# Kernel optimization log

Hardware: AMD Instinct MI355X
Metric: run time of the kernel (lower is better)

The kernel has to match this reference:

```python
import jax, jax.numpy as jnp
import numpy as np

D = 768
B = 32
N = 768


def setup_inputs() -> dict:
    key = jax.random.key(0)
    k1, k2, k3, k4 = jax.random.split(key, 4)
    stdv = 1.0 / np.sqrt(D)
    X = jax.random.normal(k1, (B, N, D), dtype=jnp.float32)
    adj = jax.random.uniform(k2, (B, N, N), dtype=jnp.float32)
    W_l = jax.random.uniform(k3, (D, D), dtype=jnp.float32, minval=-stdv, maxval=stdv)
    W_l1 = jax.random.uniform(k4, (D, D), dtype=jnp.float32, minval=-stdv, maxval=stdv)
    return {"X": X, "adj": adj, "W_l": W_l, "W_l1": W_l1}


def _row_normalize(adj):
    # rowsum^-1 with inf -> 0 (rows summing to zero stay zero)
    rowsum = adj.sum(axis=-1, keepdims=True)  # [B, N, 1]
    r_inv = jnp.where(rowsum == 0, 0.0, 1.0 / rowsum)
    return adj * r_inv


def reference(X, adj, W_l, W_l1):
    # X: [B, N, D], adj: [B, N, N]
    adj_n = _row_normalize(adj)
    e1 = jnp.einsum('bnd,de->bne', X, W_l1)        # message transform
    e11 = jnp.einsum('bnm,bmd->bnd', adj_n, e1)    # aggregate
    X1 = jnp.einsum('bnd,de->bne', X, W_l)         # self transform
    h = X1 + e11
    return jax.nn.leaky_relu(h, negative_slope=0.01)
```

## Files before the change

kernel.cpp:

```cpp
#include <hip/hip_runtime.h>
#include <hip/hip_bf16.h>
#include <cstdint>
#include <cstddef>

#define BN_ROWS 24576
#define DD 768
#define BE (768*768)
#define BM 192
#define BK 32

typedef __attribute__((ext_vector_type(8))) short bf16x8;
typedef __attribute__((ext_vector_type(4))) float f32x4;
typedef __attribute__((ext_vector_type(8))) unsigned short u16x8;

static __device__ __forceinline__ unsigned short f2bf(float f) {
  unsigned int u = __builtin_bit_cast(unsigned int, f);
  unsigned int lsb = (u >> 16) & 1u;
  u += 0x7fffu + lsb;
  return (unsigned short)(u >> 16);
}
static __device__ __forceinline__ unsigned short f2bfv(float f) {
  __hip_bfloat16 h = __float2bfloat16(f);
  return __builtin_bit_cast(unsigned short, h);
}
static __device__ __forceinline__ bf16x8 cvt8(float4 u, float4 w) {
  bf16x8 o;
  o[0] = (short)f2bfv(u.x); o[1] = (short)f2bfv(u.y);
  o[2] = (short)f2bfv(u.z); o[3] = (short)f2bfv(u.w);
  o[4] = (short)f2bfv(w.x); o[5] = (short)f2bfv(w.y);
  o[6] = (short)f2bfv(w.z); o[7] = (short)f2bfv(w.w);
  return o;
}
static __device__ __forceinline__ u16x8 pack8s(float4 a, float4 b, float sc) {
  u16x8 o;
  o[0] = f2bfv(a.x * sc); o[1] = f2bfv(a.y * sc);
  o[2] = f2bfv(a.z * sc); o[3] = f2bfv(a.w * sc);
  o[4] = f2bfv(b.x * sc); o[5] = f2bfv(b.y * sc);
  o[6] = f2bfv(b.z * sc); o[7] = f2bfv(b.w * sc);
  return o;
}


#define P_AN 3072
#define P_FL 288

__global__ __launch_bounds__(256) void prep(const float* __restrict__ adj,
                                            const float* __restrict__ Wl,
                                            const float* __restrict__ Wl1,
                                            unsigned short* __restrict__ adjnb,
                                            unsigned short* __restrict__ WlT,
                                            unsigned short* __restrict__ Wl1T) {
  const int bid = blockIdx.x;
  if (bid < P_AN) {
    const int w = threadIdx.x >> 6;
    const int hl = (threadIdx.x >> 5) & 1;
    const int l = threadIdx.x & 31;
    const int row = bid * 8 + w * 2 + hl;
    const float4* a = reinterpret_cast<const float4*>(adj + (size_t)row * DD);
    float4 v[6];
    #pragma unroll
    for (int i = 0; i < 3; ++i) {
      int u = l + i * 32;
      v[2 * i]     = a[u * 2];
      v[2 * i + 1] = a[u * 2 + 1];
    }
    float s = 0.f;
    #pragma unroll
    for (int i = 0; i < 6; ++i) s += (v[i].x + v[i].y) + (v[i].z + v[i].w);
    #pragma unroll
    for (int off = 16; off; off >>= 1) s += __shfl_xor(s, off);
    float rinv = (s == 0.f) ? 0.f : 1.f / s;
    u16x8* o = reinterpret_cast<u16x8*>(adjnb + (size_t)row * DD);
    #pragma unroll
    for (int i = 0; i < 3; ++i)
      o[l + i * 32] = pack8s(v[2 * i], v[2 * i + 1], rinv);
  } else {
    const int b2 = bid - P_AN;
    const bool isWl = b2 < P_FL;
    const int b3 = isWl ? b2 : b2 - P_FL;
    const float* src = isWl ? Wl : Wl1;
    unsigned short* dst = isWl ? WlT : Wl1T;
    const int wg = b3 * 4 + (threadIdx.x >> 6);
    const int lane = threadIdx.x & 63;
    const int d0 = (wg % 96) * 8;
    const int e = (wg / 96) * 64 + lane;
    u16x8 o;
    #pragma unroll
    for (int j = 0; j < 8; ++j)
      o[j] = f2bf(src[(size_t)(d0 + j) * DD + e]);
    const int base = ((e >> 4) * 24 + (d0 >> 5)) * 512
                   + ((e & 15) + (((d0 >> 3) & 3) << 4)) * 8;
    *reinterpret_cast<u16x8*>(dst + base) = o;
  }
}

__global__ __launch_bounds__(256, 2) void e1w(
    const float* __restrict__ X,
    const unsigned short* __restrict__ Wl1T,
    const unsigned short* __restrict__ WlT,
    unsigned short* __restrict__ e1T,
    unsigned short* __restrict__ X1f)
{
  __shared__ char smem[2 * 12288];
  constexpr int NT = 24;
  const int tid = threadIdx.x, lane = tid & 63;
  const int wid = tid >> 6;
  const int wr = wid >> 1, wc = wid & 1;

  const int logical = (blockIdx.x & 7) * 128 + (blockIdx.x >> 3);
  const int mt = logical >> 3, nt = logical & 7;
  const int b = mt >> 2;
  const float* Ag = X + (size_t)mt * BM * DD;
  const unsigned short* Bfl = (nt < 4) ? Wl1T : WlT;
  const int colblk0 = (nt & 3) * 12 + wc * 6;

  const int r_in = lane >> 2;
  const int s_in = lane & 3;

  float4 aR[3][2];
  auto issueA = [&](int s) {
    int kk = s < NT ? s : 0;
    #pragma unroll
    for (int i = 0; i < 3; ++i) {
      int row = (wid * 3 + i) * 16 + r_in;
      int slot = s_in ^ ((row >> 1) & 3);
      const float4* p = reinterpret_cast<const float4*>(
          Ag + (size_t)row * DD + kk * BK + slot * 8);
      aR[i][0] = p[0];
      aR[i][1] = p[1];
    }
  };
  auto writeA = [&](int s) {
    const int buf = (s & 1) * 12288;
    #pragma unroll
    for (int i = 0; i < 3; ++i)
      *reinterpret_cast<bf16x8*>(smem + buf + (wid * 3 + i) * 1024 + lane * 16) =
          cvt8(aR[i][0], aR[i][1]);
  };
  auto loadB = [&](int s, bf16x8* dst) {
    int kk = s < NT ? s : 0;
    #pragma unroll
    for (int ni = 0; ni < 6; ++ni)
      dst[ni] = *reinterpret_cast<const bf16x8*>(
          Bfl + ((colblk0 + ni) * 24 + kk) * 512 + lane * 8);
  };

  const int ks = lane >> 4;
  auto rdA = [&](int off, int row) -> bf16x8 {
    int slot = ks ^ ((row >> 1) & 3);
    return *reinterpret_cast<const bf16x8*>(smem + off + row * 64 + slot * 16);
  };

  f32x4 acc[6][6] = {};
  const int arow = wr * 96 + (lane & 15);
  bf16x8 bA[6], bB[6];

  auto body = [&](int bufo, bf16x8* bfr) {
    #pragma unroll
    for (int mh = 0; mh < 2; ++mh) {
      bf16x8 a[3];
      #pragma unroll
      for (int i = 0; i < 3; ++i) a[i] = rdA(bufo, arow + mh * 48 + i * 16);
      __builtin_amdgcn_s_setprio(1);
      #pragma unroll
      for (int mi = 0; mi < 3; ++mi)
        #pragma unroll
        for (int ni = 0; ni < 6; ++ni)
          acc[mh * 3 + mi][ni] = __builtin_amdgcn_mfma_f32_16x16x32_bf16(
              a[mi], bfr[ni], acc[mh * 3 + mi][ni], 0, 0, 0);
      __builtin_amdgcn_s_setprio(0);
    }
  };

  issueA(0);
  asm volatile("s_waitcnt vmcnt(0)" ::: "memory");
  writeA(0);
  loadB(0, bA);
  issueA(1);
  asm volatile("s_waitcnt lgkmcnt(0)" ::: "memory");
  __builtin_amdgcn_s_barrier();

  for (int t = 0; t < NT; t += 2) {
    loadB(t + 1, bB);
    body(0, bA);
    asm volatile("s_waitcnt vmcnt(6)" ::: "memory");
    writeA(t + 1);
    issueA(t + 2);
    asm volatile("s_waitcnt lgkmcnt(0)" ::: "memory");
    __builtin_amdgcn_s_barrier();

    loadB(t + 2, bA);
    body(12288, bB);
    asm volatile("s_waitcnt vmcnt(6)" ::: "memory");
    writeA(t + 2);
    issueA(t + 3);
    asm volatile("s_waitcnt lgkmcnt(0)" ::: "memory");
    __builtin_amdgcn_s_barrier();
  }
  asm volatile("s_waitcnt vmcnt(0)" ::: "memory");

  const int l15 = lane & 15;
  if (nt < 4) {
    unsigned short* ob = e1T + (size_t)b * BE;
    const int m0 = (mt & 3) * BM + wr * 96 + (lane >> 4) * 4;
    #pragma unroll
    for (int mi = 0; mi < 6; ++mi)
      #pragma unroll
      for (int ni = 0; ni < 6; ++ni) {
        int m = m0 + mi * 16;
        int cb = nt * 12 + wc * 6 + ni;
        int fa = (cb * 24 + (m >> 5)) * 512
               + (l15 + (((m >> 3) & 3) << 4)) * 8 + (m & 7);
        f32x4 v = acc[mi][ni];
        ushort4 o;
        o.x = f2bf(v[0]); o.y = f2bf(v[1]); o.z = f2bf(v[2]); o.w = f2bf(v[3]);
        *reinterpret_cast<ushort4*>(ob + fa) = o;
      }
  } else {
    const int flat = b * 16 + (mt & 3) * 4 + (nt - 4);
    ushort4* o4 = reinterpret_cast<ushort4*>(X1f) + (size_t)flat * 36 * 256 + tid;
    #pragma unroll
    for (int mi = 0; mi < 6; ++mi)
      #pragma unroll
      for (int ni = 0; ni < 6; ++ni) {
        f32x4 v = acc[mi][ni];
        ushort4 o;
        o.x = f2bf(v[0]); o.y = f2bf(v[1]); o.z = f2bf(v[2]); o.w = f2bf(v[3]);
        o4[(mi * 6 + ni) * 256] = o;
      }
  }
}

__global__ __launch_bounds__(256, 2) void gemm_bg(
    const unsigned short* __restrict__ adjnb,
    const unsigned short* __restrict__ e1T,
    const unsigned short* __restrict__ X1f,
    float* __restrict__ out)
{
  __shared__ char smem[24576];
  constexpr int NT = 24;
  const int tid = threadIdx.x, lane = tid & 63;
  const int wid = tid >> 6;
  const int wr = wid >> 1, wc = wid & 1;

  const int logical = (blockIdx.x & 7) * 64 + (blockIdx.x >> 3);
  const int b = logical >> 4;
  const int r = logical & 15;
  const int mt = r >> 2, nt = r & 3;
  const size_t bo = (size_t)b * BE;
  const unsigned short* A0 = adjnb + bo + (size_t)mt * BM * DD;
  const unsigned short* B0 = e1T + bo;

  const int r_in = lane >> 2;
  const int s_in = lane & 3;
  const int colblk0 = nt * 12 + wc * 6;

  auto stage = [&](int s) {
    int kk = s < NT ? s : 0;
    const int buf = (s & 1) * 12288;
    #pragma unroll
    for (int i = 0; i < 3; ++i) {
      int chunk = wid * 3 + i;
      int row = chunk * 16 + r_in;
      int slot = s_in ^ ((row >> 1) & 3);
      const unsigned short* src = A0 + (size_t)row * DD + kk * BK + slot * 8;
      __builtin_amdgcn_global_load_lds(
          (const __attribute__((address_space(1))) void*)src,
          (__attribute__((address_space(3))) void*)(smem + buf + chunk * 1024),
          16, 0, 0);
    }
  };
  auto loadB = [&](int s, bf16x8* dst) {
    int kk = s < NT ? s : 0;
    #pragma unroll
    for (int ni = 0; ni < 6; ++ni)
      dst[ni] = *reinterpret_cast<const bf16x8*>(
          B0 + ((colblk0 + ni) * 24 + kk) * 512 + lane * 8);
  };

  const int ks = lane >> 4;
  auto rdA = [&](int off, int row) -> bf16x8 {
    int slot = ks ^ ((row >> 1) & 3);
    return *reinterpret_cast<const bf16x8*>(smem + off + row * 64 + slot * 16);
  };

  f32x4 acc[6][6] = {};
  const int arow = wr * 96 + (lane & 15);
  bf16x8 bA[6], bB[6];

  auto body = [&](int bufo, bf16x8* bfr) {
    #pragma unroll
    for (int mh = 0; mh < 2; ++mh) {
      bf16x8 a[3];
      #pragma unroll
      for (int i = 0; i < 3; ++i) a[i] = rdA(bufo, arow + mh * 48 + i * 16);
      __builtin_amdgcn_s_setprio(1);
      #pragma unroll
      for (int mi = 0; mi < 3; ++mi)
        #pragma unroll
        for (int ni = 0; ni < 6; ++ni)
          acc[mh * 3 + mi][ni] = __builtin_amdgcn_mfma_f32_16x16x32_bf16(
              a[mi], bfr[ni], acc[mh * 3 + mi][ni], 0, 0, 0);
      __builtin_amdgcn_s_setprio(0);
    }
  };

  stage(0); loadB(0, bA);
  for (int t = 0; t < NT; t += 2) {
    asm volatile("s_waitcnt vmcnt(6)" ::: "memory");
    __builtin_amdgcn_s_barrier();
    stage(t + 1); loadB(t + 1, bB);
    body(0, bA);
    asm volatile("s_waitcnt vmcnt(6)" ::: "memory");
    __builtin_amdgcn_s_barrier();
    stage(t + 2); loadB(t + 2, bA);
    body(12288, bB);
  }
  asm volatile("s_waitcnt vmcnt(0)" ::: "memory");

  float* ob = out + bo;
  const int m0 = mt * BM + wr * 96 + (lane >> 4) * 4;
  const int l15 = lane & 15;
  const int flat = b * 16 + mt * 4 + nt;
  const ushort4* x4 = reinterpret_cast<const ushort4*>(X1f) + (size_t)flat * 36 * 256 + tid;
  #pragma unroll
  for (int mi = 0; mi < 6; ++mi)
    #pragma unroll
    for (int ni = 0; ni < 6; ++ni) {
      int m = m0 + mi * 16;
      int n = nt * 192 + wc * 96 + ni * 16 + l15;
      ushort4 xi = x4[(mi * 6 + ni) * 256];
      f32x4 v = acc[mi][ni];
      float x1v[4];
      x1v[0] = __builtin_bit_cast(float, (unsigned int)xi.x << 16);
      x1v[1] = __builtin_bit_cast(float, (unsigned int)xi.y << 16);
      x1v[2] = __builtin_bit_cast(float, (unsigned int)xi.z << 16);
      x1v[3] = __builtin_bit_cast(float, (unsigned int)xi.w << 16);
      #pragma unroll
      for (int j = 0; j < 4; ++j) {
        float x = v[j] + x1v[j];
        ob[(size_t)(m + j) * DD + n] = x > 0.f ? x : 0.01f * x;
      }
    }
}


extern "C" void kernel_launch(void* const* d_in, const int* in_sizes, int n_in,
                              void* d_out, int out_size, void* d_ws, size_t ws_size,
                              hipStream_t stream) {
  const float* X   = (const float*)d_in[0];
  const float* adj = (const float*)d_in[1];
  const float* Wl  = (const float*)d_in[2];
  const float* Wl1 = (const float*)d_in[3];
  float* out = (float*)d_out;

  char* ws = (char*)d_ws;
  const size_t SZ = (size_t)BN_ROWS * DD * 2;
  unsigned short* e1T   = (unsigned short*)(ws);
  unsigned short* adjnb = (unsigned short*)(ws + SZ);
  unsigned short* X1f   = (unsigned short*)(ws + 2 * SZ);
  unsigned short* WlT   = (unsigned short*)(ws + 3 * SZ);
  unsigned short* Wl1T  = (unsigned short*)(ws + 3 * SZ + (size_t)BE * 2);

  prep<<<P_AN + 2 * P_FL, 256, 0, stream>>>(adj, Wl, Wl1, adjnb, WlT, Wl1T);
  e1w<<<1024, 256, 0, stream>>>(X, Wl1T, WlT, e1T, X1f);
  gemm_bg<<<512, 256, 0, stream>>>(adjnb, e1T, X1f, out);
}
```

Measured before the change: 154.1 us.

## Fuse adjacency normalization into X-GEMM launch and stage weights via LDS

Adjacency row normalization moves out of the prep kernel and into extra blocks of the e1w GEMM launch, so the bandwidth-bound normalization can overlap with the compute-bound GEMM. The weight transpose becomes a small tiled LDS transpose into a plain row-major layout. In the GEMM, the B operand now goes through LDS with direct global-to-LDS loads and a swizzled layout, replacing per-wave fragment loads from a pre-swizzled global layout. This doubles the shared-memory footprint and changes the pipeline to a single buffer per iteration with new wait counts, which could affect occupancy and the correctness of synchronization.

```diff
diff --git a/kernel.cpp b/kernel.cpp
--- a/kernel.cpp
+++ b/kernel.cpp
@@ -8,6 +8,8 @@
 #define BE (768*768)
 #define BM 192
 #define BK 32
+#define ABUF 12288
+#define BUFSZ 24576
 
 typedef __attribute__((ext_vector_type(8))) short bf16x8;
 typedef __attribute__((ext_vector_type(4))) float f32x4;
@@ -41,21 +43,52 @@
 }
 
 
-#define P_AN 3072
-#define P_FL 288
-
-__global__ __launch_bounds__(256) void prep(const float* __restrict__ adj,
-                                            const float* __restrict__ Wl,
-                                            const float* __restrict__ Wl1,
-                                            unsigned short* __restrict__ adjnb,
-                                            unsigned short* __restrict__ WlT,
-                                            unsigned short* __restrict__ Wl1T) {
+__global__ __launch_bounds__(256) void prepW(const float* __restrict__ Wl,
+                                             const float* __restrict__ Wl1,
+                                             unsigned short* __restrict__ WlT,
+                                             unsigned short* __restrict__ Wl1T) {
+  __shared__ float tile[64][65];
+  const int tr = blockIdx.x / 12, tc = blockIdx.x % 12;
+  const int c = threadIdx.x & 63, r0 = threadIdx.x >> 6;
+  const float* srcs[2] = {Wl, Wl1};
+  unsigned short* dsts[2] = {WlT, Wl1T};
+  #pragma unroll
+  for (int m = 0; m < 2; ++m) {
+    const float* src = srcs[m];
+    #pragma unroll
+    for (int i = 0; i < 16; ++i) {
+      int r = r0 + i * 4;
+      tile[r][c] = src[(size_t)(tr * 64 + r) * DD + tc * 64 + c];
+    }
+    __syncthreads();
+    unsigned short* dst = dsts[m];
+    #pragma unroll
+    for (int i = 0; i < 16; ++i) {
+      int r2 = r0 + i * 4;
+      dst[(size_t)(tc * 64 + r2) * DD + tr * 64 + c] = f2bf(tile[c][r2]);
+    }
+    __syncthreads();
+  }
+}
+
+__global__ __launch_bounds__(256, 2) void e1w(
+    const float* __restrict__ X,
+    const float* __restrict__ adj,
+    const unsigned short* __restrict__ Wl1T,
+    const unsigned short* __restrict__ WlT,
+    unsigned short* __restrict__ e1T,
+    unsigned short* __restrict__ X1f,
+    unsigned short* __restrict__ adjnb)
+{
+  __shared__ char smem[2 * BUFSZ];
   const int bid = blockIdx.x;
-  if (bid < P_AN) {
-    const int w = threadIdx.x >> 6;
-    const int hl = (threadIdx.x >> 5) & 1;
-    const int l = threadIdx.x & 31;
-    const int row = bid * 8 + w * 2 + hl;
+  const int tid = threadIdx.x, lane = tid & 63;
+
+  if (bid >= 1024) {
+    const int w = tid >> 6;
+    const int hl = (tid >> 5) & 1;
+    const int l = tid & 31;
+    const int row = (bid - 1024) * 8 + w * 2 + hl;
     const float4* a = reinterpret_cast<const float4*>(adj + (size_t)row * DD);
     float4 v[6];
     #pragma unroll
@@ -74,45 +107,19 @@
     #pragma unroll
     for (int i = 0; i < 3; ++i)
       o[l + i * 32] = pack8s(v[2 * i], v[2 * i + 1], rinv);
-  } else {
-    const int b2 = bid - P_AN;
-    const bool isWl = b2 < P_FL;
-    const int b3 = isWl ? b2 : b2 - P_FL;
-    const float* src = isWl ? Wl : Wl1;
-    unsigned short* dst = isWl ? WlT : Wl1T;
-    const int wg = b3 * 4 + (threadIdx.x >> 6);
-    const int lane = threadIdx.x & 63;
-    const int d0 = (wg % 96) * 8;
-    const int e = (wg / 96) * 64 + lane;
-    u16x8 o;
-    #pragma unroll
-    for (int j = 0; j < 8; ++j)
-      o[j] = f2bf(src[(size_t)(d0 + j) * DD + e]);
-    const int base = ((e >> 4) * 24 + (d0 >> 5)) * 512
-                   + ((e & 15) + (((d0 >> 3) & 3) << 4)) * 8;
-    *reinterpret_cast<u16x8*>(dst + base) = o;
-  }
-}
-
-__global__ __launch_bounds__(256, 2) void e1w(
-    const float* __restrict__ X,
-    const unsigned short* __restrict__ Wl1T,
-    const unsigned short* __restrict__ WlT,
-    unsigned short* __restrict__ e1T,
-    unsigned short* __restrict__ X1f)
-{
-  __shared__ char smem[2 * 12288];
+    return;
+  }
+
   constexpr int NT = 24;
-  const int tid = threadIdx.x, lane = tid & 63;
   const int wid = tid >> 6;
   const int wr = wid >> 1, wc = wid & 1;
 
-  const int logical = (blockIdx.x & 7) * 128 + (blockIdx.x >> 3);
+  const int logical = (bid & 7) * 128 + (bid >> 3);
   const int mt = logical >> 3, nt = logical & 7;
   const int b = mt >> 2;
   const float* Ag = X + (size_t)mt * BM * DD;
-  const unsigned short* Bfl = (nt < 4) ? Wl1T : WlT;
-  const int colblk0 = (nt & 3) * 12 + wc * 6;
+  const unsigned short* Bg = (nt < 4) ? (Wl1T + (size_t)nt * 192 * DD)
+                                      : (WlT + (size_t)(nt - 4) * 192 * DD);
 
   const int r_in = lane >> 2;
   const int s_in = lane & 3;
@@ -131,73 +138,72 @@
     }
   };
   auto writeA = [&](int s) {
-    const int buf = (s & 1) * 12288;
+    const int buf = (s & 1) * BUFSZ;
     #pragma unroll
     for (int i = 0; i < 3; ++i)
       *reinterpret_cast<bf16x8*>(smem + buf + (wid * 3 + i) * 1024 + lane * 16) =
           cvt8(aR[i][0], aR[i][1]);
   };
-  auto loadB = [&](int s, bf16x8* dst) {
+  auto issueB = [&](int s) {
     int kk = s < NT ? s : 0;
-    #pragma unroll
-    for (int ni = 0; ni < 6; ++ni)
-      dst[ni] = *reinterpret_cast<const bf16x8*>(
-          Bfl + ((colblk0 + ni) * 24 + kk) * 512 + lane * 8);
+    const int buf = (s & 1) * BUFSZ + ABUF;
+    #pragma unroll
+    for (int i = 0; i < 3; ++i) {
+      int c = wid * 3 + i;
+      int row = c * 16 + r_in;
+      int slot = s_in ^ ((row >> 1) & 3);
+      const unsigned short* src = Bg + (size_t)row * DD + kk * BK + slot * 8;
+      __builtin_amdgcn_global_load_lds(
+          (const __attribute__((address_space(1))) void*)src,
+          (__attribute__((address_space(3))) void*)(smem + buf + c * 1024),
+          16, 0, 0);
+    }
   };
 
   const int ks = lane >> 4;
-  auto rdA = [&](int off, int row) -> bf16x8 {
+  auto frag = [&](int off, int row) -> bf16x8 {
     int slot = ks ^ ((row >> 1) & 3);
     return *reinterpret_cast<const bf16x8*>(smem + off + row * 64 + slot * 16);
   };
 
   f32x4 acc[6][6] = {};
   const int arow = wr * 96 + (lane & 15);
-  bf16x8 bA[6], bB[6];
-
-  auto body = [&](int bufo, bf16x8* bfr) {
-    #pragma unroll
-    for (int mh = 0; mh < 2; ++mh) {
-      bf16x8 a[3];
-      #pragma unroll
-      for (int i = 0; i < 3; ++i) a[i] = rdA(bufo, arow + mh * 48 + i * 16);
-      __builtin_amdgcn_s_setprio(1);
-      #pragma unroll
-      for (int mi = 0; mi < 3; ++mi)
-        #pragma unroll
-        for (int ni = 0; ni < 6; ++ni)
-          acc[mh * 3 + mi][ni] = __builtin_amdgcn_mfma_f32_16x16x32_bf16(
-              a[mi], bfr[ni], acc[mh * 3 + mi][ni], 0, 0, 0);
-      __builtin_amdgcn_s_setprio(0);
-    }
-  };
+  const int brow = wc * 96 + (lane & 15);
 
   issueA(0);
   asm volatile("s_waitcnt vmcnt(0)" ::: "memory");
   writeA(0);
-  loadB(0, bA);
+  issueB(0);
   issueA(1);
   asm volatile("s_waitcnt lgkmcnt(0)" ::: "memory");
   __builtin_amdgcn_s_barrier();
 
-  for (int t = 0; t < NT; t += 2) {
-    loadB(t + 1, bB);
-    body(0, bA);
+  for (int t = 0; t < NT; ++t) {
     asm volatile("s_waitcnt vmcnt(6)" ::: "memory");
+    __builtin_amdgcn_s_barrier();
+    issueB(t + 1);
+
+    const int bufA = (t & 1) * BUFSZ;
+    const int bufB = bufA + ABUF;
+    bf16x8 a[6], bg[6];
+    #pragma unroll
+    for (int i = 0; i < 6; ++i) a[i] = frag(bufA, arow + i * 16);
+    #pragma unroll
+    for (int i = 0; i < 6; ++i) bg[i] = frag(bufB, brow + i * 16);
+
+    __builtin_amdgcn_s_setprio(1);
+    #pragma unroll
+    for (int ni = 0; ni < 6; ++ni)
+      #pragma unroll
+      for (int mi = 0; mi < 6; ++mi)
+        acc[mi][ni] = __builtin_amdgcn_mfma_f32_16x16x32_bf16(a[mi], bg[ni], acc[mi][ni], 0, 0, 0);
+    __builtin_amdgcn_s_setprio(0);
+
+    asm volatile("s_waitcnt vmcnt(3)" ::: "memory");
     writeA(t + 1);
     issueA(t + 2);
     asm volatile("s_waitcnt lgkmcnt(0)" ::: "memory");
-    __builtin_amdgcn_s_barrier();
-
-    loadB(t + 2, bA);
-    body(12288, bB);
-    asm volatile("s_waitcnt vmcnt(6)" ::: "memory");
-    writeA(t + 2);
-    issueA(t + 3);
-    asm volatile("s_waitcnt lgkmcnt(0)" ::: "memory");
-    __builtin_amdgcn_s_barrier();
-  }
-  asm volatile("s_waitcnt vmcnt(0)" ::: "memory");
+  }
 
   const int l15 = lane & 15;
   if (nt < 4) {
@@ -362,7 +368,7 @@
   unsigned short* WlT   = (unsigned short*)(ws + 3 * SZ);
   unsigned short* Wl1T  = (unsigned short*)(ws + 3 * SZ + (size_t)BE * 2);
 
-  prep<<<P_AN + 2 * P_FL, 256, 0, stream>>>(adj, Wl, Wl1, adjnb, WlT, Wl1T);
-  e1w<<<1024, 256, 0, stream>>>(X, Wl1T, WlT, e1T, X1f);
+  prepW<<<144, 256, 0, stream>>>(Wl, Wl1, WlT, Wl1T);
+  e1w<<<4096, 256, 0, stream>>>(X, adj, Wl1T, WlT, e1T, X1f, adjnb);
   gemm_bg<<<512, 256, 0, stream>>>(adjnb, e1T, X1f, out);
 }
```

After: 162.1 us. +5.2%, slower.
